# Kernel tuning notes

Hardware: AMD Instinct MI355X
Metric: run time of the kernel (lower is better)

The kernel has to match this reference:

```python
import jax, jax.numpy as jnp
import numpy as np

H = 768  # bert-base hidden size; match MLP width = 2*H = 1536


def setup_inputs() -> dict:
    key = jax.random.key(0)
    ks = jax.random.split(key, 6)
    B, S = 2, 256
    std = 0.02  # TruncatedNormal(stddev=initializer_range)
    return {
        "hidden": jax.random.normal(ks[0], (B, S, H), dtype=jnp.float32),
        "w_start": jax.random.normal(ks[1], (H, 1), dtype=jnp.float32) * std,
        "b_start": jnp.zeros((1,), jnp.float32),
        "w_end": jax.random.normal(ks[2], (H, 1), dtype=jnp.float32) * std,
        "b_end": jnp.zeros((1,), jnp.float32),
        "w1": jax.random.normal(ks[3], (2 * H, 2 * H), dtype=jnp.float32) * std,
        "b1": jnp.zeros((2 * H,), jnp.float32),
        "w2": jax.random.normal(ks[4], (2 * H, 1), dtype=jnp.float32) * std,
        "b2": jnp.zeros((1,), jnp.float32),
    }


def reference(hidden, w_start, b_start, w_end, b_end, w1, b1, w2, b2):
    # hidden: [B, S, H] = BERT sequence output (dropout disabled at inference)
    start_logits = hidden @ w_start + b_start  # [B, S, 1]
    end_logits = hidden @ w_end + b_end        # [B, S, 1]

    # Pairwise span features: concat(row_i, col_j) along last dim, fed to dense1.
    # concat([row, col]) @ w1 == row @ w1[:H] + col @ w1[H:], so we split w1 and
    # broadcast-add instead of materializing the [B,S,S,2H] concat tile.
    row_proj = hidden @ w1[:H]   # [B, S, 2H] (start-token contribution)
    col_proj = hidden @ w1[H:]   # [B, S, 2H] (end-token contribution)
    pre = row_proj[:, :, None, :] + col_proj[:, None, :, :] + b1  # [B, S, S, 2H]
    act = jax.nn.gelu(pre, approximate=False)  # keras 'gelu' is exact
    match_logits = act @ w2 + b2  # [B, S, S, 1]
    return start_logits, end_logits, match_logits
```

## Files before the change

kernel.cpp:

```cpp
#include <hip/hip_runtime.h>
#include <stdint.h>

typedef __attribute__((ext_vector_type(8))) __bf16 bf16x8;
typedef __attribute__((ext_vector_type(4))) float  floatx4;
typedef __attribute__((ext_vector_type(4))) unsigned int uint4v;
typedef __attribute__((ext_vector_type(2))) unsigned int uint2v;
typedef __attribute__((ext_vector_type(4))) float  float4v;

__device__ __forceinline__ unsigned short f2bf(float f) {
  union { float f; unsigned int u; } x; x.f = f;
  unsigned int r = x.u + 0x7fffu + ((x.u >> 16) & 1u);
  return (unsigned short)(r >> 16);
}

__global__ __launch_bounds__(256) void logits_init_kernel(
    const float* __restrict__ hidden, const float* __restrict__ w_start,
    const float* __restrict__ b_start, const float* __restrict__ w_end,
    const float* __restrict__ b_end, const float* __restrict__ b2,
    float* __restrict__ out) {
  if (blockIdx.x >= 32) {
    float v = b2[0];
    int idx = ((blockIdx.x - 32) * 256 + threadIdx.x) * 4;
    *(float4v*)(out + 1024 + idx) = float4v{v, v, v, v};
    return;
  }
  const int tid  = threadIdx.x;
  const int lane = tid & 63;
  const int wv   = tid >> 6;
  const int wg   = blockIdx.x * 4 + wv;

  float wsv[12], wev[12];
#pragma unroll
  for (int t = 0; t < 12; ++t) {
    wsv[t] = w_start[lane + 64 * t];
    wev[t] = w_end[lane + 64 * t];
  }
  const float bs = b_start[0];
  const float be = b_end[0];

#pragma unroll
  for (int r = 0; r < 4; ++r) {
    int row = wg * 4 + r;
    const float* h = hidden + (size_t)row * 768;
    float ps = 0.f, pe = 0.f;
#pragma unroll
    for (int t = 0; t < 12; ++t) {
      float hv = h[lane + 64 * t];
      ps += hv * wsv[t];
      pe += hv * wev[t];
    }
#pragma unroll
    for (int off = 32; off >= 1; off >>= 1) {
      ps += __shfl_xor(ps, off, 64);
      pe += __shfl_xor(pe, off, 64);
    }
    if (lane == 0) { out[row] = ps + bs; out[512 + row] = pe + be; }
  }
}

__global__ __launch_bounds__(256) void proj_kernel(
    const float* __restrict__ hidden, const float* __restrict__ w1,
    const float* __restrict__ b1, unsigned short* __restrict__ wsR,
    unsigned short* __restrict__ wsC) {
  __shared__ short As[4 * 32 * 8];
  __shared__ short Bs[4 * 64 * 8];

  const int tid  = threadIdx.x;
  const int lane = tid & 63;
  const int wave = tid >> 6;
  const int wr = wave >> 1, wc = wave & 1;
  const int m0 = blockIdx.y * 32;
  const int n0g = blockIdx.x * 64;
  const bool isR = (n0g < 1536);
  const int kbase = isR ? 0 : 768;
  const int n0 = isR ? n0g : (n0g - 1536);
  const int q = lane >> 4, l15 = lane & 15;

  floatx4 acc0 = {}, acc1 = {};

  const int a_row = tid >> 3;
  const int a_s   = tid & 7;
  const int b_n   = tid & 63;
  const int b_kg  = tid >> 6;

  const float* hrow = hidden + (size_t)(m0 + a_row) * 768 + a_s * 4;
  const float* bcol = w1 + (size_t)(kbase + b_kg * 8) * 1536 + n0 + b_n;

  float4v hv = *(const float4v*)(hrow);
  float bv[8];
#pragma unroll
  for (int a = 0; a < 8; ++a) bv[a] = bcol[(size_t)a * 1536];

  const int aq = a_s >> 1;
  const int aj = (a_s & 1) * 4;

  for (int ko = 0; ko < 768; ko += 32) {
    uint2v au;
    au[0] = (unsigned int)f2bf(hv[0]) | ((unsigned int)f2bf(hv[1]) << 16);
    au[1] = (unsigned int)f2bf(hv[2]) | ((unsigned int)f2bf(hv[3]) << 16);
    *(uint2v*)(&As[(aq * 32 + a_row) * 8 + aj]) = au;
    uint4v pv;
#pragma unroll
    for (int a = 0; a < 4; ++a) {
      unsigned int lo = f2bf(bv[2 * a]);
      unsigned int hi = f2bf(bv[2 * a + 1]);
      pv[a] = lo | (hi << 16);
    }
    *(uint4v*)(&Bs[(b_kg * 64 + b_n) * 8]) = pv;
    __syncthreads();

    if (ko + 32 < 768) {
      hv = *(const float4v*)(hrow + ko + 32);
      const float* bp = bcol + (size_t)(ko + 32) * 1536;
#pragma unroll
      for (int a = 0; a < 8; ++a) bv[a] = bp[(size_t)a * 1536];
    }

    bf16x8 af  = *(const bf16x8*)(&As[(q * 32 + 16 * wr + l15) * 8]);
    bf16x8 bg0 = *(const bf16x8*)(&Bs[(q * 64 + 32 * wc + l15) * 8]);
    bf16x8 bg1 = *(const bf16x8*)(&Bs[(q * 64 + 32 * wc + 16 + l15) * 8]);
    acc0 = __builtin_amdgcn_mfma_f32_16x16x32_bf16(af, bg0, acc0, 0, 0, 0);
    acc1 = __builtin_amdgcn_mfma_f32_16x16x32_bf16(af, bg1, acc1, 0, 0, 0);
    __syncthreads();
  }

  unsigned short* outp = isR ? wsR : wsC;
#pragma unroll
  for (int ni = 0; ni < 2; ++ni) {
    const floatx4& ac = ni ? acc1 : acc0;
    int col = n0 + 32 * wc + 16 * ni + l15;
    float bias = isR ? b1[col] : 0.0f;
#pragma unroll
    for (int r = 0; r < 4; ++r) {
      int rowg = m0 + 16 * wr + q * 4 + r;
      outp[(size_t)rowg * 1536 + col] = f2bf(ac[r] + bias);
    }
  }
}

__global__ __launch_bounds__(256) void match_kernel(
    const unsigned short* __restrict__ wsR,
    const unsigned short* __restrict__ wsC,
    const float* __restrict__ w2,
    float* __restrict__ outm) {
  __shared__ unsigned short Rs[16 * 264];
  __shared__ unsigned short Cs[16 * 264];

  const int tid = threadIdx.x;
  const int jt = blockIdx.x, it = blockIdx.y;
  const int bz = blockIdx.z >> 1, kh = blockIdx.z & 1;
  const int i = tid >> 4, j = tid & 15;

  constexpr float C0 = 0.39103831f;
  constexpr float C1 = -0.05415410f;
  constexpr float C2 = 0.00461682f;
  constexpr float C3 = -1.51033e-4f;

  float a0 = 0.f, a1 = 0.f, a2 = 0.f, a3 = 0.f;

  const int srow = tid >> 4;
  const int scc  = tid & 15;

  const float* w2h = w2 + kh * 768;

  for (int kc = 0; kc < 3; ++kc) {
    const int Kb = kh * 768 + kc * 256;
    {
      const unsigned short* rg = wsR + (size_t)(bz * 256 + it * 16 + srow) * 1536 + Kb + scc * 16;
      const unsigned short* cg = wsC + (size_t)(bz * 256 + jt * 16 + srow) * 1536 + Kb + scc * 16;
      uint4v rv0 = *(const uint4v*)rg;
      uint4v rv1 = *(const uint4v*)(rg + 8);
      uint4v cv0 = *(const uint4v*)cg;
      uint4v cv1 = *(const uint4v*)(cg + 8);
      unsigned short* rd = &Rs[srow * 264 + scc * 16];
      unsigned short* cd = &Cs[srow * 264 + scc * 16];
      *(uint4v*)(rd)     = rv0;
      *(uint4v*)(rd + 8) = rv1;
      *(uint4v*)(cd)     = cv0;
      *(uint4v*)(cd + 8) = cv1;
    }
    __syncthreads();

    const unsigned short* rp = &Rs[i * 264];
    const unsigned short* cp = &Cs[j * 264];
    const float* wq = w2h + kc * 256;
#pragma unroll 2
    for (int k = 0; k < 256; k += 8) {
      uint4v rv = *(const uint4v*)(rp + k);
      uint4v cv = *(const uint4v*)(cp + k);
#pragma unroll
      for (int a = 0; a < 4; ++a) {
        union { unsigned int u; float f; } rl, rh, cl, ch;
        rl.u = rv[a] << 16; rh.u = rv[a] & 0xffff0000u;
        cl.u = cv[a] << 16; ch.u = cv[a] & 0xffff0000u;
        float w_lo = wq[k + 2 * a];
        float w_hi = wq[k + 2 * a + 1];
        {
          float x  = rl.f + cl.f;
          float xc = fminf(fmaxf(x, -3.5f), 3.5f);
          float u  = xc * xc;
          float p  = fmaf(u, fmaf(u, fmaf(u, C3, C2), C1), C0);
          float g  = x * fmaf(xc, p, 0.5f);
          if (a == 0) a0 = fmaf(g, w_lo, a0);
          else if (a == 1) a1 = fmaf(g, w_lo, a1);
          else if (a == 2) a2 = fmaf(g, w_lo, a2);
          else a3 = fmaf(g, w_lo, a3);
        }
        {
          float x  = rh.f + ch.f;
          float xc = fminf(fmaxf(x, -3.5f), 3.5f);
          float u  = xc * xc;
          float p  = fmaf(u, fmaf(u, fmaf(u, C3, C2), C1), C0);
          float g  = x * fmaf(xc, p, 0.5f);
          if (a == 0) a0 = fmaf(g, w_hi, a0);
          else if (a == 1) a1 = fmaf(g, w_hi, a1);
          else if (a == 2) a2 = fmaf(g, w_hi, a2);
          else a3 = fmaf(g, w_hi, a3);
        }
      }
    }
    __syncthreads();
  }

  float acc = (a0 + a1) + (a2 + a3);
  size_t idx = ((size_t)bz * 256 + it * 16 + i) * 256 + (jt * 16 + j);
  unsafeAtomicAdd(&outm[idx], acc);
}

extern "C" void kernel_launch(void* const* d_in, const int* in_sizes, int n_in,
                              void* d_out, int out_size, void* d_ws, size_t ws_size,
                              hipStream_t stream) {
  const float* hidden  = (const float*)d_in[0];
  const float* w_start = (const float*)d_in[1];
  const float* b_start = (const float*)d_in[2];
  const float* w_end   = (const float*)d_in[3];
  const float* b_end   = (const float*)d_in[4];
  const float* w1      = (const float*)d_in[5];
  const float* b1      = (const float*)d_in[6];
  const float* w2      = (const float*)d_in[7];
  const float* b2      = (const float*)d_in[8];

  float* out = (float*)d_out;
  char* ws = (char*)d_ws;
  unsigned short* wsR = (unsigned short*)(ws);
  unsigned short* wsC = (unsigned short*)(ws + 1572864);

  logits_init_kernel<<<dim3(160), dim3(256), 0, stream>>>(
      hidden, w_start, b_start, w_end, b_end, b2, out);
  proj_kernel<<<dim3(48, 16), dim3(256), 0, stream>>>(hidden, w1, b1, wsR, wsC);
  match_kernel<<<dim3(16, 16, 4), dim3(256), 0, stream>>>(wsR, wsC, w2, out + 1024);
}
```

Measured before the change: 138.7 us.

## Register-block match kernel 2x1, stage fp32 tiles and w2 in LDS, split K four ways

The match kernel now has each thread compute two output rows against one column. This halves the column-tile LDS reads per GELU evaluation. The bf16 tiles are unpacked to fp32 once when loaded into shared memory, and w2 is staged in LDS, so the inner loop no longer does bit-unpacking or global w2 loads. K is split four ways instead of two, keeping the block count the same while doubling the atomic adds per output. The cost is more LDS use and extra atomic traffic.

After: 137.2 us. Within noise of the previous version (-1.1%).

```diff
diff --git a/kernel.cpp b/kernel.cpp
--- a/kernel.cpp
+++ b/kernel.cpp
@@ -143,12 +143,13 @@
     const unsigned short* __restrict__ wsC,
     const float* __restrict__ w2,
     float* __restrict__ outm) {
-  __shared__ unsigned short Rs[16 * 264];
-  __shared__ unsigned short Cs[16 * 264];
+  __shared__ float Rs[32 * 132];
+  __shared__ float Cs[16 * 132];
+  __shared__ float Ws[128];
 
   const int tid = threadIdx.x;
   const int jt = blockIdx.x, it = blockIdx.y;
-  const int bz = blockIdx.z >> 1, kh = blockIdx.z & 1;
+  const int bz = blockIdx.z >> 2, kh = blockIdx.z & 3;
   const int i = tid >> 4, j = tid & 15;
 
   constexpr float C0 = 0.39103831f;
@@ -156,75 +157,103 @@
   constexpr float C2 = 0.00461682f;
   constexpr float C3 = -1.51033e-4f;
 
-  float a0 = 0.f, a1 = 0.f, a2 = 0.f, a3 = 0.f;
-
-  const int srow = tid >> 4;
-  const int scc  = tid & 15;
-
-  const float* w2h = w2 + kh * 768;
+  float a00 = 0.f, a01 = 0.f, a10 = 0.f, a11 = 0.f;
+
+  const int rrow = tid >> 3, rko = (tid & 7) * 16;
+  const int crow = tid >> 4, cko = (tid & 15) * 8;
 
   for (int kc = 0; kc < 3; ++kc) {
-    const int Kb = kh * 768 + kc * 256;
+    const int Kb = kh * 384 + kc * 128;
     {
-      const unsigned short* rg = wsR + (size_t)(bz * 256 + it * 16 + srow) * 1536 + Kb + scc * 16;
-      const unsigned short* cg = wsC + (size_t)(bz * 256 + jt * 16 + srow) * 1536 + Kb + scc * 16;
+      const unsigned short* rg = wsR + (size_t)(bz * 256 + it * 32 + rrow) * 1536 + Kb + rko;
+      const unsigned short* cg = wsC + (size_t)(bz * 256 + jt * 16 + crow) * 1536 + Kb + cko;
       uint4v rv0 = *(const uint4v*)rg;
       uint4v rv1 = *(const uint4v*)(rg + 8);
-      uint4v cv0 = *(const uint4v*)cg;
-      uint4v cv1 = *(const uint4v*)(cg + 8);
-      unsigned short* rd = &Rs[srow * 264 + scc * 16];
-      unsigned short* cd = &Cs[srow * 264 + scc * 16];
-      *(uint4v*)(rd)     = rv0;
-      *(uint4v*)(rd + 8) = rv1;
-      *(uint4v*)(cd)     = cv0;
-      *(uint4v*)(cd + 8) = cv1;
-    }
-    __syncthreads();
-
-    const unsigned short* rp = &Rs[i * 264];
-    const unsigned short* cp = &Cs[j * 264];
-    const float* wq = w2h + kc * 256;
+      uint4v cv  = *(const uint4v*)cg;
+      float* rd = &Rs[rrow * 132 + rko];
+      float* cd = &Cs[crow * 132 + cko];
+      union { unsigned int u; float f; } lo, hi;
+#pragma unroll
+      for (int h = 0; h < 2; ++h) {
+        uint4v rv = h ? rv1 : rv0;
+        float4v f0, f1;
+        lo.u = rv[0] << 16; hi.u = rv[0] & 0xffff0000u; f0[0] = lo.f; f0[1] = hi.f;
+        lo.u = rv[1] << 16; hi.u = rv[1] & 0xffff0000u; f0[2] = lo.f; f0[3] = hi.f;
+        lo.u = rv[2] << 16; hi.u = rv[2] & 0xffff0000u; f1[0] = lo.f; f1[1] = hi.f;
+        lo.u = rv[3] << 16; hi.u = rv[3] & 0xffff0000u; f1[2] = lo.f; f1[3] = hi.f;
+        *(float4v*)(rd + 8 * h)     = f0;
+        *(float4v*)(rd + 8 * h + 4) = f1;
+      }
+      {
+        float4v g0, g1;
+        lo.u = cv[0] << 16; hi.u = cv[0] & 0xffff0000u; g0[0] = lo.f; g0[1] = hi.f;
+        lo.u = cv[1] << 16; hi.u = cv[1] & 0xffff0000u; g0[2] = lo.f; g0[3] = hi.f;
+        lo.u = cv[2] << 16; hi.u = cv[2] & 0xffff0000u; g1[0] = lo.f; g1[1] = hi.f;
+        lo.u = cv[3] << 16; hi.u = cv[3] & 0xffff0000u; g1[2] = lo.f; g1[3] = hi.f;
+        *(float4v*)(cd)     = g0;
+        *(float4v*)(cd + 4) = g1;
+      }
+      if (tid < 128) Ws[tid] = w2[Kb + tid];
+    }
+    __syncthreads();
+
+    const float* rp0 = &Rs[(2 * i) * 132];
+    const float* rp1 = rp0 + 132;
+    const float* cp  = &Cs[j * 132];
 #pragma unroll 2
-    for (int k = 0; k < 256; k += 8) {
-      uint4v rv = *(const uint4v*)(rp + k);
-      uint4v cv = *(const uint4v*)(cp + k);
-#pragma unroll
-      for (int a = 0; a < 4; ++a) {
-        union { unsigned int u; float f; } rl, rh, cl, ch;
-        rl.u = rv[a] << 16; rh.u = rv[a] & 0xffff0000u;
-        cl.u = cv[a] << 16; ch.u = cv[a] & 0xffff0000u;
-        float w_lo = wq[k + 2 * a];
-        float w_hi = wq[k + 2 * a + 1];
-        {
-          float x  = rl.f + cl.f;
-          float xc = fminf(fmaxf(x, -3.5f), 3.5f);
-          float u  = xc * xc;
-          float p  = fmaf(u, fmaf(u, fmaf(u, C3, C2), C1), C0);
-          float g  = x * fmaf(xc, p, 0.5f);
-          if (a == 0) a0 = fmaf(g, w_lo, a0);
-          else if (a == 1) a1 = fmaf(g, w_lo, a1);
-          else if (a == 2) a2 = fmaf(g, w_lo, a2);
-          else a3 = fmaf(g, w_lo, a3);
-        }
-        {
-          float x  = rh.f + ch.f;
-          float xc = fminf(fmaxf(x, -3.5f), 3.5f);
-          float u  = xc * xc;
-          float p  = fmaf(u, fmaf(u, fmaf(u, C3, C2), C1), C0);
-          float g  = x * fmaf(xc, p, 0.5f);
-          if (a == 0) a0 = fmaf(g, w_hi, a0);
-          else if (a == 1) a1 = fmaf(g, w_hi, a1);
-          else if (a == 2) a2 = fmaf(g, w_hi, a2);
-          else a3 = fmaf(g, w_hi, a3);
+    for (int k = 0; k < 128; k += 8) {
+      float4v r0a = *(const float4v*)(rp0 + k);
+      float4v r0b = *(const float4v*)(rp0 + k + 4);
+      float4v r1a = *(const float4v*)(rp1 + k);
+      float4v r1b = *(const float4v*)(rp1 + k + 4);
+      float4v ca  = *(const float4v*)(cp + k);
+      float4v cb  = *(const float4v*)(cp + k + 4);
+      float4v wa  = *(const float4v*)(&Ws[k]);
+      float4v wb  = *(const float4v*)(&Ws[k + 4]);
+#pragma unroll
+      for (int d = 0; d < 4; ++d) {
+        {
+          float x  = r0a[d] + ca[d];
+          float xc = fminf(fmaxf(x, -3.5f), 3.5f);
+          float u  = xc * xc;
+          float p  = fmaf(u, fmaf(u, fmaf(u, C3, C2), C1), C0);
+          float g  = x * fmaf(xc, p, 0.5f);
+          a00 = fmaf(g, wa[d], a00);
+        }
+        {
+          float x  = r1a[d] + ca[d];
+          float xc = fminf(fmaxf(x, -3.5f), 3.5f);
+          float u  = xc * xc;
+          float p  = fmaf(u, fmaf(u, fmaf(u, C3, C2), C1), C0);
+          float g  = x * fmaf(xc, p, 0.5f);
+          a10 = fmaf(g, wa[d], a10);
+        }
+        {
+          float x  = r0b[d] + cb[d];
+          float xc = fminf(fmaxf(x, -3.5f), 3.5f);
+          float u  = xc * xc;
+          float p  = fmaf(u, fmaf(u, fmaf(u, C3, C2), C1), C0);
+          float g  = x * fmaf(xc, p, 0.5f);
+          a01 = fmaf(g, wb[d], a01);
+        }
+        {
+          float x  = r1b[d] + cb[d];
+          float xc = fminf(fmaxf(x, -3.5f), 3.5f);
+          float u  = xc * xc;
+          float p  = fmaf(u, fmaf(u, fmaf(u, C3, C2), C1), C0);
+          float g  = x * fmaf(xc, p, 0.5f);
+          a11 = fmaf(g, wb[d], a11);
         }
       }
     }
     __syncthreads();
   }
 
-  float acc = (a0 + a1) + (a2 + a3);
-  size_t idx = ((size_t)bz * 256 + it * 16 + i) * 256 + (jt * 16 + j);
-  unsafeAtomicAdd(&outm[idx], acc);
+  int gi = bz * 256 + it * 32 + 2 * i;
+  int gj = jt * 16 + j;
+  float* o0 = outm + (size_t)gi * 256 + gj;
+  unsafeAtomicAdd(o0,       a00 + a01);
+  unsafeAtomicAdd(o0 + 256, a10 + a11);
 }
 
 extern "C" void kernel_launch(void* const* d_in, const int* in_sizes, int n_in,
@@ -248,5 +277,5 @@
   logits_init_kernel<<<dim3(160), dim3(256), 0, stream>>>(
       hidden, w_start, b_start, w_end, b_end, b2, out);
   proj_kernel<<<dim3(48, 16), dim3(256), 0, stream>>>(hidden, w1, b1, wsR, wsC);
-  match_kernel<<<dim3(16, 16, 4), dim3(256), 0, stream>>>(wsR, wsC, w2, out + 1024);
-}
+  match_kernel<<<dim3(16, 8, 8), dim3(256), 0, stream>>>(wsR, wsC, w2, out + 1024);
+}
```

## Read match operands directly from global memory with register prefetch, stage w2 in LDS

Applied to the files above, without the earlier changes.

The match kernel no longer stages 16-row tiles of R and C projections through shared memory with per-chunk barriers. Each thread now streams its own row and column vectors straight from global memory (through L1/L2), using a one-step register prefetch, and w2 is loaded once into shared memory for vectorized reads. This removes the chunk barriers and LDS copies. In exchange, every thread issues its own global loads: each R and C row is re-read by 16 threads, and the lanes of a wave access memory with a 1536-element stride between rows, so access coalescing is poorer.

Measured after the change: 148.1 us. 1.07x slower.

```diff
diff --git a/kernel.cpp b/kernel.cpp
--- a/kernel.cpp
+++ b/kernel.cpp
@@ -143,8 +143,7 @@
     const unsigned short* __restrict__ wsC,
     const float* __restrict__ w2,
     float* __restrict__ outm) {
-  __shared__ unsigned short Rs[16 * 264];
-  __shared__ unsigned short Cs[16 * 264];
+  __shared__ float Ws[768];
 
   const int tid = threadIdx.x;
   const int jt = blockIdx.x, it = blockIdx.y;
@@ -156,74 +155,65 @@
   constexpr float C2 = 0.00461682f;
   constexpr float C3 = -1.51033e-4f;
 
+  Ws[tid]       = w2[kh * 768 + tid];
+  Ws[tid + 256] = w2[kh * 768 + tid + 256];
+  Ws[tid + 512] = w2[kh * 768 + tid + 512];
+  __syncthreads();
+
+  const int gi = bz * 256 + it * 16 + i;
+  const int gj = jt * 16 + j;
+  const unsigned short* rp = wsR + (size_t)gi * 1536 + kh * 768;
+  const unsigned short* cp = wsC + (size_t)(bz * 256 + gj) * 1536 + kh * 768;
+
   float a0 = 0.f, a1 = 0.f, a2 = 0.f, a3 = 0.f;
 
-  const int srow = tid >> 4;
-  const int scc  = tid & 15;
-
-  const float* w2h = w2 + kh * 768;
-
-  for (int kc = 0; kc < 3; ++kc) {
-    const int Kb = kh * 768 + kc * 256;
-    {
-      const unsigned short* rg = wsR + (size_t)(bz * 256 + it * 16 + srow) * 1536 + Kb + scc * 16;
-      const unsigned short* cg = wsC + (size_t)(bz * 256 + jt * 16 + srow) * 1536 + Kb + scc * 16;
-      uint4v rv0 = *(const uint4v*)rg;
-      uint4v rv1 = *(const uint4v*)(rg + 8);
-      uint4v cv0 = *(const uint4v*)cg;
-      uint4v cv1 = *(const uint4v*)(cg + 8);
-      unsigned short* rd = &Rs[srow * 264 + scc * 16];
-      unsigned short* cd = &Cs[srow * 264 + scc * 16];
-      *(uint4v*)(rd)     = rv0;
-      *(uint4v*)(rd + 8) = rv1;
-      *(uint4v*)(cd)     = cv0;
-      *(uint4v*)(cd + 8) = cv1;
-    }
-    __syncthreads();
-
-    const unsigned short* rp = &Rs[i * 264];
-    const unsigned short* cp = &Cs[j * 264];
-    const float* wq = w2h + kc * 256;
-#pragma unroll 2
-    for (int k = 0; k < 256; k += 8) {
-      uint4v rv = *(const uint4v*)(rp + k);
-      uint4v cv = *(const uint4v*)(cp + k);
-#pragma unroll
-      for (int a = 0; a < 4; ++a) {
-        union { unsigned int u; float f; } rl, rh, cl, ch;
-        rl.u = rv[a] << 16; rh.u = rv[a] & 0xffff0000u;
-        cl.u = cv[a] << 16; ch.u = cv[a] & 0xffff0000u;
-        float w_lo = wq[k + 2 * a];
-        float w_hi = wq[k + 2 * a + 1];
-        {
-          float x  = rl.f + cl.f;
-          float xc = fminf(fmaxf(x, -3.5f), 3.5f);
-          float u  = xc * xc;
-          float p  = fmaf(u, fmaf(u, fmaf(u, C3, C2), C1), C0);
-          float g  = x * fmaf(xc, p, 0.5f);
-          if (a == 0) a0 = fmaf(g, w_lo, a0);
-          else if (a == 1) a1 = fmaf(g, w_lo, a1);
-          else if (a == 2) a2 = fmaf(g, w_lo, a2);
-          else a3 = fmaf(g, w_lo, a3);
-        }
-        {
-          float x  = rh.f + ch.f;
-          float xc = fminf(fmaxf(x, -3.5f), 3.5f);
-          float u  = xc * xc;
-          float p  = fmaf(u, fmaf(u, fmaf(u, C3, C2), C1), C0);
-          float g  = x * fmaf(xc, p, 0.5f);
-          if (a == 0) a0 = fmaf(g, w_hi, a0);
-          else if (a == 1) a1 = fmaf(g, w_hi, a1);
-          else if (a == 2) a2 = fmaf(g, w_hi, a2);
-          else a3 = fmaf(g, w_hi, a3);
-        }
+  uint4v rv = *(const uint4v*)(rp);
+  uint4v cv = *(const uint4v*)(cp);
+
+  for (int k = 0; k < 768; k += 8) {
+    uint4v rn = rv, cn = cv;
+    if (k + 8 < 768) {
+      rn = *(const uint4v*)(rp + k + 8);
+      cn = *(const uint4v*)(cp + k + 8);
+    }
+    float4v wa = *(const float4v*)(&Ws[k]);
+    float4v wb = *(const float4v*)(&Ws[k + 4]);
+#pragma unroll
+    for (int a = 0; a < 4; ++a) {
+      union { unsigned int u; float f; } rl, rh, cl, ch;
+      rl.u = rv[a] << 16; rh.u = rv[a] & 0xffff0000u;
+      cl.u = cv[a] << 16; ch.u = cv[a] & 0xffff0000u;
+      float w_lo = (a < 2) ? wa[2 * a]     : wb[2 * a - 4];
+      float w_hi = (a < 2) ? wa[2 * a + 1] : wb[2 * a - 3];
+      {
+        float x  = rl.f + cl.f;
+        float xc = fminf(fmaxf(x, -3.5f), 3.5f);
+        float u  = xc * xc;
+        float p  = fmaf(u, fmaf(u, fmaf(u, C3, C2), C1), C0);
+        float g  = x * fmaf(xc, p, 0.5f);
+        if (a == 0) a0 = fmaf(g, w_lo, a0);
+        else if (a == 1) a1 = fmaf(g, w_lo, a1);
+        else if (a == 2) a2 = fmaf(g, w_lo, a2);
+        else a3 = fmaf(g, w_lo, a3);
       }
-    }
-    __syncthreads();
+      {
+        float x  = rh.f + ch.f;
+        float xc = fminf(fmaxf(x, -3.5f), 3.5f);
+        float u  = xc * xc;
+        float p  = fmaf(u, fmaf(u, fmaf(u, C3, C2), C1), C0);
+        float g  = x * fmaf(xc, p, 0.5f);
+        if (a == 0) a0 = fmaf(g, w_hi, a0);
+        else if (a == 1) a1 = fmaf(g, w_hi, a1);
+        else if (a == 2) a2 = fmaf(g, w_hi, a2);
+        else a3 = fmaf(g, w_hi, a3);
+      }
+    }
+    rv = rn;
+    cv = cn;
   }
 
   float acc = (a0 + a1) + (a2 + a3);
-  size_t idx = ((size_t)bz * 256 + it * 16 + i) * 256 + (jt * 16 + j);
+  size_t idx = ((size_t)gi) * 256 + gj;
   unsafeAtomicAdd(&outm[idx], acc);
 }
 
```
